# Optimization experiments

Measured on AMD Instinct MI355X. Metric: run time of the kernel, lower is better.

## Reference

```python
import jax, jax.numpy as jnp
import numpy as np

CAPACITY_FACTOR = 1.25

def setup_inputs() -> dict:
    key = jax.random.key(0)
    ks = jax.random.split(key, 6)
    B, S, D, H, E = 4, 2048, 1024, 2048, 8
    x = jax.random.normal(ks[0], (B, S, D), dtype=jnp.float32)
    Wg = jax.random.normal(ks[1], (D, E), dtype=jnp.float32) / np.float32(np.sqrt(D))
    bg = jnp.zeros((E,), dtype=jnp.float32)
    W1 = jax.random.normal(ks[2], (E, H, D), dtype=jnp.float32) / np.float32(np.sqrt(H))
    W2 = jax.random.normal(ks[3], (E, D, H), dtype=jnp.float32) / np.float32(np.sqrt(D))
    W3 = jax.random.normal(ks[4], (E, D, H), dtype=jnp.float32) / np.float32(np.sqrt(D))
    return {"x": x, "Wg": Wg, "bg": bg, "W1": W1, "W2": W2, "W3": W3, "deterministic": 1}


def reference(x, Wg, bg, W1, W2, W3, deterministic):
    # deterministic=True path: no gate noise, no dropout (rate=0 anyway).
    b, s, d = x.shape
    E = W1.shape[0]
    xt = x.reshape(-1, d)                      # [N, d]
    N = xt.shape[0]
    cap = int(N / E * CAPACITY_FACTOR)

    logits = xt @ Wg + bg                      # [N, E]
    eid = jnp.argmax(logits, axis=1)           # [N] assigned expert (top-1)
    onehot = jax.nn.one_hot(eid, E, dtype=xt.dtype)
    # 0-based arrival position of each token within its expert's queue
    pos = (jnp.sum(jnp.cumsum(onehot, axis=0) * onehot, axis=1)).astype(jnp.int32) - 1
    valid = pos < cap                          # capacity mask (pos >= 0 always)
    slot = jnp.where(valid, pos, cap)          # overflow tokens -> dummy slot `cap`

    # Dispatch: scatter tokens into [E, cap+1, d]; slots unique among valid tokens
    buf = jnp.zeros((E, cap + 1, d), dtype=xt.dtype).at[eid, slot].set(xt)
    binp = buf[:, :cap]                        # [E, cap, d] (dummy slot dropped)

    # Grouped SwiGLU FFN per expert
    h = jax.nn.silu(jnp.einsum('ecd,edh->ech', binp, W2)) * jnp.einsum('ecd,edh->ech', binp, W3)
    bout = jnp.einsum('ech,ehd->ecd', h, W1)   # [E, cap, d]

    # Combine: gather each token's expert output; overflow tokens read zero row
    bout = jnp.concatenate([bout, jnp.zeros((E, 1, d), dtype=bout.dtype)], axis=1)
    eout = bout[eid, slot]                     # [N, d]

    weights = jax.nn.softmax(logits, axis=-1)
    gate_w = jnp.take_along_axis(weights, eid[:, None], axis=1)  # [N, 1]
    out = (gate_w * eout).reshape(b, s, d)
    return out
```

## Files before the change

### kernel.cpp

```cpp
#include <hip/hip_runtime.h>

#define N_TOK 8192
#define D_DIM 1024
#define H_DIM 2048
#define E_NUM 8
#define CAP   1280

typedef __attribute__((ext_vector_type(8))) short bf16x8;
typedef __attribute__((ext_vector_type(8))) unsigned short u16x8;
typedef __attribute__((ext_vector_type(4))) float f32x4;

__device__ inline unsigned short f2bf(float f) {
  unsigned u = __float_as_uint(f);
  u += 0x7fffu + ((u >> 16) & 1u);
  return (unsigned short)(u >> 16);
}

__device__ inline void vm_drain() {
  asm volatile("s_waitcnt vmcnt(0)" ::: "memory");
}

__global__ __launch_bounds__(256) void transpose_cvt(const float* __restrict__ src,
                                                     unsigned short* __restrict__ dst,
                                                     int R, int C) {
  __shared__ float tile[64][33];
  const int b = blockIdx.z;
  src += (size_t)b * R * C;
  dst += (size_t)b * R * C;
  const int c0 = blockIdx.x * 32, r0 = blockIdx.y * 64;
  const int tx = threadIdx.x & 31, ty = threadIdx.x >> 5;
#pragma unroll
  for (int i = 0; i < 8; ++i)
    tile[ty + i * 8][tx] = src[(size_t)(r0 + ty + i * 8) * C + c0 + tx];
  __syncthreads();
  const int rp = threadIdx.x & 31;
  const int cb = threadIdx.x >> 5;
#pragma unroll
  for (int it = 0; it < 4; ++it) {
    const int c = cb + it * 8;
    unsigned short v[2] = {f2bf(tile[2 * rp][c]), f2bf(tile[2 * rp + 1][c])};
    *reinterpret_cast<unsigned*>(dst + (size_t)(c0 + c) * R + r0 + 2 * rp) =
        *reinterpret_cast<unsigned*>(v);
  }
}

__global__ __launch_bounds__(256) void gate_kernel(const float* __restrict__ x,
                                                   const float* __restrict__ Wg,
                                                   const float* __restrict__ bg,
                                                   int* __restrict__ eid,
                                                   float* __restrict__ gatew) {
  __shared__ float wg[E_NUM][D_DIM];
  const int tid = threadIdx.x;
  for (int i = tid; i < D_DIM * E_NUM; i += 256) {
    int d = i >> 3, e = i & 7;
    wg[e][d] = Wg[i];
  }
  __syncthreads();
  const int w = tid >> 6, l = tid & 63;
  const int t = blockIdx.x * 4 + w;
  const float* xr = x + (size_t)t * D_DIM;
  float acc[8] = {0, 0, 0, 0, 0, 0, 0, 0};
#pragma unroll
  for (int i = 0; i < D_DIM / 64; ++i) {
    float xv = xr[l + 64 * i];
#pragma unroll
    for (int e = 0; e < 8; ++e) acc[e] += xv * wg[e][l + 64 * i];
  }
#pragma unroll
  for (int off = 32; off >= 1; off >>= 1) {
#pragma unroll
    for (int e = 0; e < 8; ++e) acc[e] += __shfl_xor(acc[e], off);
  }
  if (l == 0) {
    float best = -1e30f;
    int bi = 0;
#pragma unroll
    for (int e = 0; e < 8; ++e) {
      acc[e] += bg[e];
      if (acc[e] > best) { best = acc[e]; bi = e; }
    }
    float s = 0.f;
#pragma unroll
    for (int e = 0; e < 8; ++e) s += __expf(acc[e] - best);
    eid[t] = bi;
    gatew[t] = 1.f / s;
  }
}

__global__ void init_tok(int* __restrict__ tok_of) {
  int i = blockIdx.x * 256 + threadIdx.x;
  if (i < E_NUM * CAP) tok_of[i] = -1;
}

__global__ void scan_kernel(const int* __restrict__ eid, int* __restrict__ slot,
                            int* __restrict__ tok_of) {
  __shared__ int se[N_TOK];
  const int tid = threadIdx.x;
  for (int i = tid; i < N_TOK; i += 256) se[i] = eid[i];
  __syncthreads();
  if (tid >= 64) return;
  int counts[8] = {0, 0, 0, 0, 0, 0, 0, 0};
  const unsigned long long lower = (tid == 0) ? 0ull : ((1ull << tid) - 1ull);
  for (int base = 0; base < N_TOK; base += 64) {
    const int t = base + tid;
    const int e = se[t];
    int rank = 0;
#pragma unroll
    for (int ee = 0; ee < 8; ++ee) {
      unsigned long long m = __ballot(e == ee);
      if (e == ee) rank = counts[ee] + __popcll(m & lower);
      counts[ee] += __popcll(m);
    }
    slot[t] = rank < CAP ? rank : CAP;
    if (rank < CAP) tok_of[e * CAP + rank] = t;
  }
}

__global__ __launch_bounds__(256) void scatter_kernel(const float* __restrict__ x,
                                                      const int* __restrict__ tok_of,
                                                      unsigned short* __restrict__ binp) {
  const int row = blockIdx.x * 4 + (threadIdx.x >> 6);
  const int l = threadIdx.x & 63;
  const int t = tok_of[row];
  unsigned short* dst = binp + (size_t)row * D_DIM;
  if (t >= 0) {
    const float* src = x + (size_t)t * D_DIM;
#pragma unroll
    for (int i = 0; i < 4; ++i) {
      const int d = (i * 64 + l) * 4;
      float4 v = *reinterpret_cast<const float4*>(src + d);
      unsigned short r[4] = {f2bf(v.x), f2bf(v.y), f2bf(v.z), f2bf(v.w)};
      *reinterpret_cast<uint2*>(dst + d) = *reinterpret_cast<uint2*>(r);
    }
  } else {
    uint2 z = {0u, 0u};
#pragma unroll
    for (int i = 0; i < 4; ++i) {
      const int d = (i * 64 + l) * 4;
      *reinterpret_cast<uint2*>(dst + d) = z;
    }
  }
}

__device__ inline void stage_tile_async(const unsigned short* __restrict__ g, int ldg, int k0,
                                        unsigned short* lds, int w, int l) {
  const int gcol = (l & 7) ^ (l >> 3);
  const unsigned short* gsrc = g + (size_t)(w * 32 + (l >> 3)) * ldg + k0 + gcol * 8;
#pragma unroll
  for (int it = 0; it < 4; ++it) {
    __builtin_amdgcn_global_load_lds(
        (const __attribute__((address_space(1))) unsigned int*)(gsrc + (size_t)(it * 8) * ldg),
        (__attribute__((address_space(3))) unsigned int*)(lds + (w * 32 + it * 8) * 64),
        16, 0, 0);
  }
}

__device__ inline bf16x8 lds_frag(const unsigned short* lds, int row, int c16) {
  return *reinterpret_cast<const bf16x8*>(lds + row * 64 + (c16 ^ (row & 7)) * 8);
}

__global__ __launch_bounds__(256, 2) void ffn1_kernel(const unsigned short* __restrict__ binp,
                                                      const unsigned short* __restrict__ w2t,
                                                      const unsigned short* __restrict__ w3t,
                                                      unsigned short* __restrict__ hbuf) {
  __shared__ unsigned short sA[128 * 64], sB2[128 * 64], sB3[128 * 64];
  const int e = blockIdx.z;
  const unsigned short* A  = binp + (size_t)e * CAP * D_DIM + (size_t)blockIdx.y * 128 * D_DIM;
  const unsigned short* B2 = w2t + (size_t)e * H_DIM * D_DIM + (size_t)blockIdx.x * 128 * D_DIM;
  const unsigned short* B3 = w3t + (size_t)e * H_DIM * D_DIM + (size_t)blockIdx.x * 128 * D_DIM;
  unsigned short* H = hbuf + (size_t)e * CAP * H_DIM;
  const int tid = threadIdx.x;
  const int l = tid & 63;
  const int w = tid >> 6, wr = w >> 1, wc = w & 1;
  f32x4 acc2[4][4] = {};
  f32x4 acc3[4][4] = {};
  for (int kt = 0; kt < D_DIM / 64; ++kt) {
    __syncthreads();
    stage_tile_async(A, D_DIM, kt * 64, sA, w, l);
    stage_tile_async(B2, D_DIM, kt * 64, sB2, w, l);
    stage_tile_async(B3, D_DIM, kt * 64, sB3, w, l);
    vm_drain();
    __syncthreads();
#pragma unroll
    for (int kk = 0; kk < 2; ++kk) {
      const int c16 = kk * 4 + (l >> 4);
      bf16x8 af[4], b2f[4], b3f[4];
#pragma unroll
      for (int f = 0; f < 4; ++f) {
        af[f] = lds_frag(sA, wr * 64 + f * 16 + (l & 15), c16);
        b2f[f] = lds_frag(sB2, wc * 64 + f * 16 + (l & 15), c16);
        b3f[f] = lds_frag(sB3, wc * 64 + f * 16 + (l & 15), c16);
      }
#pragma unroll
      for (int fm = 0; fm < 4; ++fm)
#pragma unroll
        for (int fn = 0; fn < 4; ++fn) {
          acc2[fm][fn] = __builtin_amdgcn_mfma_f32_16x16x32_bf16(af[fm], b2f[fn], acc2[fm][fn], 0, 0, 0);
          acc3[fm][fn] = __builtin_amdgcn_mfma_f32_16x16x32_bf16(af[fm], b3f[fn], acc3[fm][fn], 0, 0, 0);
        }
    }
  }
  const int row0 = blockIdx.y * 128 + wr * 64;
  const int col0 = blockIdx.x * 128 + wc * 64;
#pragma unroll
  for (int fm = 0; fm < 4; ++fm)
#pragma unroll
    for (int fn = 0; fn < 4; ++fn)
#pragma unroll
      for (int j = 0; j < 4; ++j) {
        const int row = row0 + fm * 16 + (l >> 4) * 4 + j;
        const int col = col0 + fn * 16 + (l & 15);
        const float v1 = acc2[fm][fn][j];
        const float v2 = acc3[fm][fn][j];
        const float hv = (v1 / (1.0f + __expf(-v1))) * v2;
        H[(size_t)row * H_DIM + col] = f2bf(hv);
      }
}

__global__ __launch_bounds__(256, 2) void ffn2_kernel(const unsigned short* __restrict__ hbuf,
                                                      const unsigned short* __restrict__ w1t,
                                                      const int* __restrict__ tok_of,
                                                      const float* __restrict__ gatew,
                                                      float* __restrict__ out) {
  __shared__ unsigned short sA[128 * 64], sB[128 * 64];
  const int e = blockIdx.z;
  const unsigned short* A = hbuf + (size_t)e * CAP * H_DIM + (size_t)blockIdx.y * 128 * H_DIM;
  const unsigned short* B = w1t + (size_t)e * D_DIM * H_DIM + (size_t)blockIdx.x * 128 * H_DIM;
  const int* tok = tok_of + e * CAP;
  const int tid = threadIdx.x;
  const int l = tid & 63;
  const int w = tid >> 6, wr = w >> 1, wc = w & 1;
  f32x4 acc[4][4] = {};
  for (int kt = 0; kt < H_DIM / 64; ++kt) {
    __syncthreads();
    stage_tile_async(A, H_DIM, kt * 64, sA, w, l);
    stage_tile_async(B, H_DIM, kt * 64, sB, w, l);
    vm_drain();
    __syncthreads();
#pragma unroll
    for (int kk = 0; kk < 2; ++kk) {
      const int c16 = kk * 4 + (l >> 4);
      bf16x8 af[4], bf[4];
#pragma unroll
      for (int f = 0; f < 4; ++f) {
        af[f] = lds_frag(sA, wr * 64 + f * 16 + (l & 15), c16);
        bf[f] = lds_frag(sB, wc * 64 + f * 16 + (l & 15), c16);
      }
#pragma unroll
      for (int fm = 0; fm < 4; ++fm)
#pragma unroll
        for (int fn = 0; fn < 4; ++fn)
          acc[fm][fn] = __builtin_amdgcn_mfma_f32_16x16x32_bf16(af[fm], bf[fn], acc[fm][fn], 0, 0, 0);
    }
  }
  const int row0 = blockIdx.y * 128 + wr * 64;
  const int col0 = blockIdx.x * 128 + wc * 64;
#pragma unroll
  for (int fm = 0; fm < 4; ++fm)
#pragma unroll
    for (int j = 0; j < 4; ++j) {
      const int row = row0 + fm * 16 + (l >> 4) * 4 + j;
      const int t = tok[row];
      if (t >= 0) {
        const float g = gatew[t];
#pragma unroll
        for (int fn = 0; fn < 4; ++fn) {
          const int col = col0 + fn * 16 + (l & 15);
          out[(size_t)t * D_DIM + col] = g * acc[fm][fn][j];
        }
      }
    }
}

__global__ __launch_bounds__(256) void zero_overflow(const int* __restrict__ slot,
                                                     float* __restrict__ out) {
  const int t = blockIdx.x * 4 + (threadIdx.x >> 6);
  if (slot[t] < CAP) return;
  const int l = threadIdx.x & 63;
  float4 z = {0.f, 0.f, 0.f, 0.f};
#pragma unroll
  for (int i = 0; i < 4; ++i)
    *reinterpret_cast<float4*>(out + (size_t)t * D_DIM + (i * 64 + l) * 4) = z;
}

extern "C" void kernel_launch(void* const* d_in, const int* in_sizes, int n_in,
                              void* d_out, int out_size, void* d_ws, size_t ws_size,
                              hipStream_t stream) {
  const float* x  = (const float*)d_in[0];
  const float* Wg = (const float*)d_in[1];
  const float* bg = (const float*)d_in[2];
  const float* W1 = (const float*)d_in[3];
  const float* W2 = (const float*)d_in[4];
  const float* W3 = (const float*)d_in[5];
  float* out = (float*)d_out;

  char* ws = (char*)d_ws;
  unsigned short* w2t = (unsigned short*)ws; ws += (size_t)E_NUM * H_DIM * D_DIM * 2;
  unsigned short* w3t = (unsigned short*)ws; ws += (size_t)E_NUM * H_DIM * D_DIM * 2;
  unsigned short* w1t = (unsigned short*)ws; ws += (size_t)E_NUM * D_DIM * H_DIM * 2;
  unsigned short* binp = (unsigned short*)ws; ws += (size_t)E_NUM * CAP * D_DIM * 2;
  unsigned short* hbuf = (unsigned short*)ws; ws += (size_t)E_NUM * CAP * H_DIM * 2;
  int* eid = (int*)ws;    ws += (size_t)N_TOK * 4;
  float* gw = (float*)ws; ws += (size_t)N_TOK * 4;
  int* slot = (int*)ws;   ws += (size_t)N_TOK * 4;
  int* tok_of = (int*)ws; ws += (size_t)E_NUM * CAP * 4;

  dim3 tb(256);
  transpose_cvt<<<dim3(H_DIM / 32, D_DIM / 64, E_NUM), tb, 0, stream>>>(W2, w2t, D_DIM, H_DIM);
  transpose_cvt<<<dim3(H_DIM / 32, D_DIM / 64, E_NUM), tb, 0, stream>>>(W3, w3t, D_DIM, H_DIM);
  transpose_cvt<<<dim3(D_DIM / 32, H_DIM / 64, E_NUM), tb, 0, stream>>>(W1, w1t, H_DIM, D_DIM);

  init_tok<<<(E_NUM * CAP + 255) / 256, 256, 0, stream>>>(tok_of);
  gate_kernel<<<N_TOK / 4, 256, 0, stream>>>(x, Wg, bg, eid, gw);
  scan_kernel<<<1, 256, 0, stream>>>(eid, slot, tok_of);
  scatter_kernel<<<E_NUM * CAP / 4, 256, 0, stream>>>(x, tok_of, binp);
  ffn1_kernel<<<dim3(H_DIM / 128, CAP / 128, E_NUM), 256, 0, stream>>>(binp, w2t, w3t, hbuf);
  ffn2_kernel<<<dim3(D_DIM / 128, CAP / 128, E_NUM), 256, 0, stream>>>(hbuf, w1t, tok_of, gw, out);
  zero_overflow<<<N_TOK / 4, 256, 0, stream>>>(slot, out);
}
```

Measured before the change: 272.7 us.

## Double-buffer LDS tiles with K=32 steps to overlap loads and MFMA

Both grouped GEMM kernels now split K into 32-wide tiles held in two LDS buffers, with a new XOR swizzle suited to the 32-column rows. The loads for the next tile are issued before the MFMAs on the current one, so global-to-LDS traffic overlaps compute instead of being drained before each step. The price is twice as many K iterations and barriers per output tile, with a shorter compute window to hide each load in.

Measured after the change: 327.8 us. 1.2x slower.

```diff
diff --git a/kernel.cpp b/kernel.cpp
--- a/kernel.cpp
+++ b/kernel.cpp
@@ -7,7 +7,6 @@
 #define CAP   1280
 
 typedef __attribute__((ext_vector_type(8))) short bf16x8;
-typedef __attribute__((ext_vector_type(8))) unsigned short u16x8;
 typedef __attribute__((ext_vector_type(4))) float f32x4;
 
 __device__ inline unsigned short f2bf(float f) {
@@ -142,28 +141,32 @@
   }
 }
 
-__device__ inline void stage_tile_async(const unsigned short* __restrict__ g, int ldg, int k0,
-                                        unsigned short* lds, int w, int l) {
-  const int gcol = (l & 7) ^ (l >> 3);
-  const unsigned short* gsrc = g + (size_t)(w * 32 + (l >> 3)) * ldg + k0 + gcol * 8;
-#pragma unroll
-  for (int it = 0; it < 4; ++it) {
+#define TILE32 (128 * 32)
+
+__device__ inline void stage_tile32(const unsigned short* __restrict__ g, int ldg, int k0,
+                                    unsigned short* lds, int w, int l) {
+  const int q = l >> 2;
+  const int gcol = (l & 3) ^ (q & 3) ^ ((q >> 2) & 3);
+  const unsigned short* gsrc = g + (size_t)(w * 32 + q) * ldg + k0 + gcol * 8;
+#pragma unroll
+  for (int it = 0; it < 2; ++it) {
     __builtin_amdgcn_global_load_lds(
-        (const __attribute__((address_space(1))) unsigned int*)(gsrc + (size_t)(it * 8) * ldg),
-        (__attribute__((address_space(3))) unsigned int*)(lds + (w * 32 + it * 8) * 64),
+        (const __attribute__((address_space(1))) unsigned int*)(gsrc + (size_t)(it * 16) * ldg),
+        (__attribute__((address_space(3))) unsigned int*)(lds + (w * 32 + it * 16) * 32),
         16, 0, 0);
   }
 }
 
-__device__ inline bf16x8 lds_frag(const unsigned short* lds, int row, int c16) {
-  return *reinterpret_cast<const bf16x8*>(lds + row * 64 + (c16 ^ (row & 7)) * 8);
+__device__ inline bf16x8 lds_frag32(const unsigned short* lds, int row, int c) {
+  const int ch = c ^ (row & 3) ^ ((row >> 2) & 3);
+  return *reinterpret_cast<const bf16x8*>(lds + row * 32 + ch * 8);
 }
 
 __global__ __launch_bounds__(256, 2) void ffn1_kernel(const unsigned short* __restrict__ binp,
                                                       const unsigned short* __restrict__ w2t,
                                                       const unsigned short* __restrict__ w3t,
                                                       unsigned short* __restrict__ hbuf) {
-  __shared__ unsigned short sA[128 * 64], sB2[128 * 64], sB3[128 * 64];
+  __shared__ unsigned short sA[2][TILE32], sB2[2][TILE32], sB3[2][TILE32];
   const int e = blockIdx.z;
   const unsigned short* A  = binp + (size_t)e * CAP * D_DIM + (size_t)blockIdx.y * 128 * D_DIM;
   const unsigned short* B2 = w2t + (size_t)e * H_DIM * D_DIM + (size_t)blockIdx.x * 128 * D_DIM;
@@ -174,32 +177,42 @@
   const int w = tid >> 6, wr = w >> 1, wc = w & 1;
   f32x4 acc2[4][4] = {};
   f32x4 acc3[4][4] = {};
-  for (int kt = 0; kt < D_DIM / 64; ++kt) {
-    __syncthreads();
-    stage_tile_async(A, D_DIM, kt * 64, sA, w, l);
-    stage_tile_async(B2, D_DIM, kt * 64, sB2, w, l);
-    stage_tile_async(B3, D_DIM, kt * 64, sB3, w, l);
+
+  stage_tile32(A, D_DIM, 0, sA[0], w, l);
+  stage_tile32(B2, D_DIM, 0, sB2[0], w, l);
+  stage_tile32(B3, D_DIM, 0, sB3[0], w, l);
+  vm_drain();
+  __syncthreads();
+
+  const int NT = D_DIM / 32;
+  int cur = 0;
+  for (int kt = 0; kt < NT; ++kt) {
+    const int nxt = cur ^ 1;
+    if (kt + 1 < NT) {
+      stage_tile32(A, D_DIM, (kt + 1) * 32, sA[nxt], w, l);
+      stage_tile32(B2, D_DIM, (kt + 1) * 32, sB2[nxt], w, l);
+      stage_tile32(B3, D_DIM, (kt + 1) * 32, sB3[nxt], w, l);
+    }
+    const int c = l >> 4;
+    bf16x8 af[4], b2f[4], b3f[4];
+#pragma unroll
+    for (int f = 0; f < 4; ++f) {
+      af[f]  = lds_frag32(sA[cur],  wr * 64 + f * 16 + (l & 15), c);
+      b2f[f] = lds_frag32(sB2[cur], wc * 64 + f * 16 + (l & 15), c);
+      b3f[f] = lds_frag32(sB3[cur], wc * 64 + f * 16 + (l & 15), c);
+    }
+#pragma unroll
+    for (int fm = 0; fm < 4; ++fm)
+#pragma unroll
+      for (int fn = 0; fn < 4; ++fn) {
+        acc2[fm][fn] = __builtin_amdgcn_mfma_f32_16x16x32_bf16(af[fm], b2f[fn], acc2[fm][fn], 0, 0, 0);
+        acc3[fm][fn] = __builtin_amdgcn_mfma_f32_16x16x32_bf16(af[fm], b3f[fn], acc3[fm][fn], 0, 0, 0);
+      }
     vm_drain();
     __syncthreads();
-#pragma unroll
-    for (int kk = 0; kk < 2; ++kk) {
-      const int c16 = kk * 4 + (l >> 4);
-      bf16x8 af[4], b2f[4], b3f[4];
-#pragma unroll
-      for (int f = 0; f < 4; ++f) {
-        af[f] = lds_frag(sA, wr * 64 + f * 16 + (l & 15), c16);
-        b2f[f] = lds_frag(sB2, wc * 64 + f * 16 + (l & 15), c16);
-        b3f[f] = lds_frag(sB3, wc * 64 + f * 16 + (l & 15), c16);
-      }
-#pragma unroll
-      for (int fm = 0; fm < 4; ++fm)
-#pragma unroll
-        for (int fn = 0; fn < 4; ++fn) {
-          acc2[fm][fn] = __builtin_amdgcn_mfma_f32_16x16x32_bf16(af[fm], b2f[fn], acc2[fm][fn], 0, 0, 0);
-          acc3[fm][fn] = __builtin_amdgcn_mfma_f32_16x16x32_bf16(af[fm], b3f[fn], acc3[fm][fn], 0, 0, 0);
-        }
-    }
-  }
+    cur = nxt;
+  }
+
   const int row0 = blockIdx.y * 128 + wr * 64;
   const int col0 = blockIdx.x * 128 + wc * 64;
 #pragma unroll
@@ -222,7 +235,7 @@
                                                       const int* __restrict__ tok_of,
                                                       const float* __restrict__ gatew,
                                                       float* __restrict__ out) {
-  __shared__ unsigned short sA[128 * 64], sB[128 * 64];
+  __shared__ unsigned short sA[2][TILE32], sB[2][TILE32];
   const int e = blockIdx.z;
   const unsigned short* A = hbuf + (size_t)e * CAP * H_DIM + (size_t)blockIdx.y * 128 * H_DIM;
   const unsigned short* B = w1t + (size_t)e * D_DIM * H_DIM + (size_t)blockIdx.x * 128 * H_DIM;
@@ -231,28 +244,37 @@
   const int l = tid & 63;
   const int w = tid >> 6, wr = w >> 1, wc = w & 1;
   f32x4 acc[4][4] = {};
-  for (int kt = 0; kt < H_DIM / 64; ++kt) {
-    __syncthreads();
-    stage_tile_async(A, H_DIM, kt * 64, sA, w, l);
-    stage_tile_async(B, H_DIM, kt * 64, sB, w, l);
+
+  stage_tile32(A, H_DIM, 0, sA[0], w, l);
+  stage_tile32(B, H_DIM, 0, sB[0], w, l);
+  vm_drain();
+  __syncthreads();
+
+  const int NT = H_DIM / 32;
+  int cur = 0;
+  for (int kt = 0; kt < NT; ++kt) {
+    const int nxt = cur ^ 1;
+    if (kt + 1 < NT) {
+      stage_tile32(A, H_DIM, (kt + 1) * 32, sA[nxt], w, l);
+      stage_tile32(B, H_DIM, (kt + 1) * 32, sB[nxt], w, l);
+    }
+    const int c = l >> 4;
+    bf16x8 af[4], bfr[4];
+#pragma unroll
+    for (int f = 0; f < 4; ++f) {
+      af[f]  = lds_frag32(sA[cur], wr * 64 + f * 16 + (l & 15), c);
+      bfr[f] = lds_frag32(sB[cur], wc * 64 + f * 16 + (l & 15), c);
+    }
+#pragma unroll
+    for (int fm = 0; fm < 4; ++fm)
+#pragma unroll
+      for (int fn = 0; fn < 4; ++fn)
+        acc[fm][fn] = __builtin_amdgcn_mfma_f32_16x16x32_bf16(af[fm], bfr[fn], acc[fm][fn], 0, 0, 0);
     vm_drain();
     __syncthreads();
-#pragma unroll
-    for (int kk = 0; kk < 2; ++kk) {
-      const int c16 = kk * 4 + (l >> 4);
-      bf16x8 af[4], bf[4];
-#pragma unroll
-      for (int f = 0; f < 4; ++f) {
-        af[f] = lds_frag(sA, wr * 64 + f * 16 + (l & 15), c16);
-        bf[f] = lds_frag(sB, wc * 64 + f * 16 + (l & 15), c16);
-      }
-#pragma unroll
-      for (int fm = 0; fm < 4; ++fm)
-#pragma unroll
-        for (int fn = 0; fn < 4; ++fn)
-          acc[fm][fn] = __builtin_amdgcn_mfma_f32_16x16x32_bf16(af[fm], bf[fn], acc[fm][fn], 0, 0, 0);
-    }
-  }
+    cur = nxt;
+  }
+
   const int row0 = blockIdx.y * 128 + wr * 64;
   const int col0 = blockIdx.x * 128 + wc * 64;
 #pragma unroll
```

## Double-buffer GEMM K-loop and interleave W2/W3 into one B operand

Applied to the files above, without the earlier changes.

Both FFN GEMMs now use double-buffered LDS tiles: the next K slice is prefetched with async global-to-LDS loads while MFMAs run on the current slice, which hides load latency behind compute. The gate and up projection weights are packed into one interleaved matrix, 64 rows of W2 followed by 64 rows of W3 per 128-row block. ffn1 therefore computes one 128x128 output tile, and the SwiGLU pairing is done through an LDS scratch exchange between wave columns. This halves ffn1's accumulator registers and doubles its grid, at the cost of an extra LDS round trip in the epilogue and more LDS per block.

Result: slower. 290.3 us (+6.4%).

```diff
diff --git a/kernel.cpp b/kernel.cpp
--- a/kernel.cpp
+++ b/kernel.cpp
@@ -7,7 +7,6 @@
 #define CAP   1280
 
 typedef __attribute__((ext_vector_type(8))) short bf16x8;
-typedef __attribute__((ext_vector_type(8))) unsigned short u16x8;
 typedef __attribute__((ext_vector_type(4))) float f32x4;
 
 __device__ inline unsigned short f2bf(float f) {
@@ -40,6 +39,32 @@
     const int c = cb + it * 8;
     unsigned short v[2] = {f2bf(tile[2 * rp][c]), f2bf(tile[2 * rp + 1][c])};
     *reinterpret_cast<unsigned*>(dst + (size_t)(c0 + c) * R + r0 + 2 * rp) =
+        *reinterpret_cast<unsigned*>(v);
+  }
+}
+
+__global__ __launch_bounds__(256) void transpose_cvt_merge(const float* __restrict__ src,
+                                                           unsigned short* __restrict__ dst,
+                                                           int R, int C, int rowoff) {
+  __shared__ float tile[64][33];
+  const int b = blockIdx.z;
+  src += (size_t)b * R * C;
+  dst += (size_t)b * 2 * C * R;
+  const int c0 = blockIdx.x * 32, r0 = blockIdx.y * 64;
+  const int tx = threadIdx.x & 31, ty = threadIdx.x >> 5;
+#pragma unroll
+  for (int i = 0; i < 8; ++i)
+    tile[ty + i * 8][tx] = src[(size_t)(r0 + ty + i * 8) * C + c0 + tx];
+  __syncthreads();
+  const int rp = threadIdx.x & 31;
+  const int cb = threadIdx.x >> 5;
+#pragma unroll
+  for (int it = 0; it < 4; ++it) {
+    const int c = cb + it * 8;
+    const int h = c0 + c;
+    const size_t drow = (size_t)(h >> 6) * 128 + (h & 63) + rowoff;
+    unsigned short v[2] = {f2bf(tile[2 * rp][c]), f2bf(tile[2 * rp + 1][c])};
+    *reinterpret_cast<unsigned*>(dst + drow * R + r0 + 2 * rp) =
         *reinterpret_cast<unsigned*>(v);
   }
 }
@@ -142,8 +167,10 @@
   }
 }
 
-__device__ inline void stage_tile_async(const unsigned short* __restrict__ g, int ldg, int k0,
-                                        unsigned short* lds, int w, int l) {
+#define TILE64 (128 * 64)
+
+__device__ inline void stage_tile(const unsigned short* __restrict__ g, int ldg, int k0,
+                                  unsigned short* lds, int w, int l) {
   const int gcol = (l & 7) ^ (l >> 3);
   const unsigned short* gsrc = g + (size_t)(w * 32 + (l >> 3)) * ldg + k0 + gcol * 8;
 #pragma unroll
@@ -160,61 +187,82 @@
 }
 
 __global__ __launch_bounds__(256, 2) void ffn1_kernel(const unsigned short* __restrict__ binp,
-                                                      const unsigned short* __restrict__ w2t,
-                                                      const unsigned short* __restrict__ w3t,
+                                                      const unsigned short* __restrict__ wq,
                                                       unsigned short* __restrict__ hbuf) {
-  __shared__ unsigned short sA[128 * 64], sB2[128 * 64], sB3[128 * 64];
-  const int e = blockIdx.z;
-  const unsigned short* A  = binp + (size_t)e * CAP * D_DIM + (size_t)blockIdx.y * 128 * D_DIM;
-  const unsigned short* B2 = w2t + (size_t)e * H_DIM * D_DIM + (size_t)blockIdx.x * 128 * D_DIM;
-  const unsigned short* B3 = w3t + (size_t)e * H_DIM * D_DIM + (size_t)blockIdx.x * 128 * D_DIM;
+  __shared__ unsigned short sb[2][2][TILE64];
+  const int e = blockIdx.z, bx = blockIdx.x, by = blockIdx.y;
+  const unsigned short* A = binp + (size_t)e * CAP * D_DIM + (size_t)by * 128 * D_DIM;
+  const unsigned short* B = wq + ((size_t)e * (H_DIM / 64) + bx) * 128 * D_DIM;
   unsigned short* H = hbuf + (size_t)e * CAP * H_DIM;
   const int tid = threadIdx.x;
   const int l = tid & 63;
   const int w = tid >> 6, wr = w >> 1, wc = w & 1;
-  f32x4 acc2[4][4] = {};
-  f32x4 acc3[4][4] = {};
-  for (int kt = 0; kt < D_DIM / 64; ++kt) {
-    __syncthreads();
-    stage_tile_async(A, D_DIM, kt * 64, sA, w, l);
-    stage_tile_async(B2, D_DIM, kt * 64, sB2, w, l);
-    stage_tile_async(B3, D_DIM, kt * 64, sB3, w, l);
+  f32x4 acc[4][4] = {};
+
+  stage_tile(A, D_DIM, 0, sb[0][0], w, l);
+  stage_tile(B, D_DIM, 0, sb[0][1], w, l);
+  vm_drain();
+  __syncthreads();
+
+  const int NT = D_DIM / 64;
+  int cur = 0;
+  for (int kt = 0; kt < NT; ++kt) {
+    const int nxt = cur ^ 1;
+    if (kt + 1 < NT) {
+      stage_tile(A, D_DIM, (kt + 1) * 64, sb[nxt][0], w, l);
+      stage_tile(B, D_DIM, (kt + 1) * 64, sb[nxt][1], w, l);
+    }
+#pragma unroll
+    for (int kk = 0; kk < 2; ++kk) {
+      const int c16 = kk * 4 + (l >> 4);
+      bf16x8 af[4], bfr[4];
+#pragma unroll
+      for (int f = 0; f < 4; ++f) {
+        af[f]  = lds_frag(sb[cur][0], wr * 64 + f * 16 + (l & 15), c16);
+        bfr[f] = lds_frag(sb[cur][1], wc * 64 + f * 16 + (l & 15), c16);
+      }
+#pragma unroll
+      for (int fm = 0; fm < 4; ++fm)
+#pragma unroll
+        for (int fn = 0; fn < 4; ++fn)
+          acc[fm][fn] = __builtin_amdgcn_mfma_f32_16x16x32_bf16(af[fm], bfr[fn], acc[fm][fn], 0, 0, 0);
+    }
     vm_drain();
     __syncthreads();
-#pragma unroll
-    for (int kk = 0; kk < 2; ++kk) {
-      const int c16 = kk * 4 + (l >> 4);
-      bf16x8 af[4], b2f[4], b3f[4];
-#pragma unroll
-      for (int f = 0; f < 4; ++f) {
-        af[f] = lds_frag(sA, wr * 64 + f * 16 + (l & 15), c16);
-        b2f[f] = lds_frag(sB2, wc * 64 + f * 16 + (l & 15), c16);
-        b3f[f] = lds_frag(sB3, wc * 64 + f * 16 + (l & 15), c16);
-      }
-#pragma unroll
-      for (int fm = 0; fm < 4; ++fm)
-#pragma unroll
-        for (int fn = 0; fn < 4; ++fn) {
-          acc2[fm][fn] = __builtin_amdgcn_mfma_f32_16x16x32_bf16(af[fm], b2f[fn], acc2[fm][fn], 0, 0, 0);
-          acc3[fm][fn] = __builtin_amdgcn_mfma_f32_16x16x32_bf16(af[fm], b3f[fn], acc3[fm][fn], 0, 0, 0);
+    cur = nxt;
+  }
+
+  float* scr = reinterpret_cast<float*>(&sb[0][0][0]);
+  if (wc == 1) {
+#pragma unroll
+    for (int fm = 0; fm < 4; ++fm)
+#pragma unroll
+      for (int fn = 0; fn < 4; ++fn)
+#pragma unroll
+        for (int j = 0; j < 4; ++j) {
+          const int r = fm * 16 + (l >> 4) * 4 + j;
+          const int c = fn * 16 + (l & 15);
+          scr[wr * 4160 + r * 65 + c] = acc[fm][fn][j];
         }
-    }
-  }
-  const int row0 = blockIdx.y * 128 + wr * 64;
-  const int col0 = blockIdx.x * 128 + wc * 64;
-#pragma unroll
-  for (int fm = 0; fm < 4; ++fm)
-#pragma unroll
-    for (int fn = 0; fn < 4; ++fn)
-#pragma unroll
-      for (int j = 0; j < 4; ++j) {
-        const int row = row0 + fm * 16 + (l >> 4) * 4 + j;
-        const int col = col0 + fn * 16 + (l & 15);
-        const float v1 = acc2[fm][fn][j];
-        const float v2 = acc3[fm][fn][j];
-        const float hv = (v1 / (1.0f + __expf(-v1))) * v2;
-        H[(size_t)row * H_DIM + col] = f2bf(hv);
-      }
+  }
+  __syncthreads();
+  if (wc == 0) {
+    const int row0 = by * 128 + wr * 64;
+    const int col0 = bx * 64;
+#pragma unroll
+    for (int fm = 0; fm < 4; ++fm)
+#pragma unroll
+      for (int fn = 0; fn < 4; ++fn)
+#pragma unroll
+        for (int j = 0; j < 4; ++j) {
+          const int r = fm * 16 + (l >> 4) * 4 + j;
+          const int c = fn * 16 + (l & 15);
+          const float v2 = acc[fm][fn][j];
+          const float v3 = scr[wr * 4160 + r * 65 + c];
+          const float hv = (v2 / (1.0f + __expf(-v2))) * v3;
+          H[(size_t)(row0 + r) * H_DIM + col0 + c] = f2bf(hv);
+        }
+  }
 }
 
 __global__ __launch_bounds__(256, 2) void ffn2_kernel(const unsigned short* __restrict__ hbuf,
@@ -222,7 +270,7 @@
                                                       const int* __restrict__ tok_of,
                                                       const float* __restrict__ gatew,
                                                       float* __restrict__ out) {
-  __shared__ unsigned short sA[128 * 64], sB[128 * 64];
+  __shared__ unsigned short sb[2][2][TILE64];
   const int e = blockIdx.z;
   const unsigned short* A = hbuf + (size_t)e * CAP * H_DIM + (size_t)blockIdx.y * 128 * H_DIM;
   const unsigned short* B = w1t + (size_t)e * D_DIM * H_DIM + (size_t)blockIdx.x * 128 * H_DIM;
@@ -231,28 +279,40 @@
   const int l = tid & 63;
   const int w = tid >> 6, wr = w >> 1, wc = w & 1;
   f32x4 acc[4][4] = {};
-  for (int kt = 0; kt < H_DIM / 64; ++kt) {
-    __syncthreads();
-    stage_tile_async(A, H_DIM, kt * 64, sA, w, l);
-    stage_tile_async(B, H_DIM, kt * 64, sB, w, l);
+
+  stage_tile(A, H_DIM, 0, sb[0][0], w, l);
+  stage_tile(B, H_DIM, 0, sb[0][1], w, l);
+  vm_drain();
+  __syncthreads();
+
+  const int NT = H_DIM / 64;
+  int cur = 0;
+  for (int kt = 0; kt < NT; ++kt) {
+    const int nxt = cur ^ 1;
+    if (kt + 1 < NT) {
+      stage_tile(A, H_DIM, (kt + 1) * 64, sb[nxt][0], w, l);
+      stage_tile(B, H_DIM, (kt + 1) * 64, sb[nxt][1], w, l);
+    }
+#pragma unroll
+    for (int kk = 0; kk < 2; ++kk) {
+      const int c16 = kk * 4 + (l >> 4);
+      bf16x8 af[4], bfr[4];
+#pragma unroll
+      for (int f = 0; f < 4; ++f) {
+        af[f]  = lds_frag(sb[cur][0], wr * 64 + f * 16 + (l & 15), c16);
+        bfr[f] = lds_frag(sb[cur][1], wc * 64 + f * 16 + (l & 15), c16);
+      }
+#pragma unroll
+      for (int fm = 0; fm < 4; ++fm)
+#pragma unroll
+        for (int fn = 0; fn < 4; ++fn)
+          acc[fm][fn] = __builtin_amdgcn_mfma_f32_16x16x32_bf16(af[fm], bfr[fn], acc[fm][fn], 0, 0, 0);
+    }
     vm_drain();
     __syncthreads();
-#pragma unroll
-    for (int kk = 0; kk < 2; ++kk) {
-      const int c16 = kk * 4 + (l >> 4);
-      bf16x8 af[4], bf[4];
-#pragma unroll
-      for (int f = 0; f < 4; ++f) {
-        af[f] = lds_frag(sA, wr * 64 + f * 16 + (l & 15), c16);
-        bf[f] = lds_frag(sB, wc * 64 + f * 16 + (l & 15), c16);
-      }
-#pragma unroll
-      for (int fm = 0; fm < 4; ++fm)
-#pragma unroll
-        for (int fn = 0; fn < 4; ++fn)
-          acc[fm][fn] = __builtin_amdgcn_mfma_f32_16x16x32_bf16(af[fm], bf[fn], acc[fm][fn], 0, 0, 0);
-    }
-  }
+    cur = nxt;
+  }
+
   const int row0 = blockIdx.y * 128 + wr * 64;
   const int col0 = blockIdx.x * 128 + wc * 64;
 #pragma unroll
@@ -295,8 +355,7 @@
   float* out = (float*)d_out;
 
   char* ws = (char*)d_ws;
-  unsigned short* w2t = (unsigned short*)ws; ws += (size_t)E_NUM * H_DIM * D_DIM * 2;
-  unsigned short* w3t = (unsigned short*)ws; ws += (size_t)E_NUM * H_DIM * D_DIM * 2;
+  unsigned short* wq  = (unsigned short*)ws; ws += (size_t)E_NUM * 2 * H_DIM * D_DIM * 2;
   unsigned short* w1t = (unsigned short*)ws; ws += (size_t)E_NUM * D_DIM * H_DIM * 2;
   unsigned short* binp = (unsigned short*)ws; ws += (size_t)E_NUM * CAP * D_DIM * 2;
   unsigned short* hbuf = (unsigned short*)ws; ws += (size_t)E_NUM * CAP * H_DIM * 2;
@@ -306,15 +365,15 @@
   int* tok_of = (int*)ws; ws += (size_t)E_NUM * CAP * 4;
 
   dim3 tb(256);
-  transpose_cvt<<<dim3(H_DIM / 32, D_DIM / 64, E_NUM), tb, 0, stream>>>(W2, w2t, D_DIM, H_DIM);
-  transpose_cvt<<<dim3(H_DIM / 32, D_DIM / 64, E_NUM), tb, 0, stream>>>(W3, w3t, D_DIM, H_DIM);
+  transpose_cvt_merge<<<dim3(H_DIM / 32, D_DIM / 64, E_NUM), tb, 0, stream>>>(W2, wq, D_DIM, H_DIM, 0);
+  transpose_cvt_merge<<<dim3(H_DIM / 32, D_DIM / 64, E_NUM), tb, 0, stream>>>(W3, wq, D_DIM, H_DIM, 64);
   transpose_cvt<<<dim3(D_DIM / 32, H_DIM / 64, E_NUM), tb, 0, stream>>>(W1, w1t, H_DIM, D_DIM);
 
   init_tok<<<(E_NUM * CAP + 255) / 256, 256, 0, stream>>>(tok_of);
   gate_kernel<<<N_TOK / 4, 256, 0, stream>>>(x, Wg, bg, eid, gw);
   scan_kernel<<<1, 256, 0, stream>>>(eid, slot, tok_of);
   scatter_kernel<<<E_NUM * CAP / 4, 256, 0, stream>>>(x, tok_of, binp);
-  ffn1_kernel<<<dim3(H_DIM / 128, CAP / 128, E_NUM), 256, 0, stream>>>(binp, w2t, w3t, hbuf);
+  ffn1_kernel<<<dim3(H_DIM / 64, CAP / 128, E_NUM), 256, 0, stream>>>(binp, wq, hbuf);
   ffn2_kernel<<<dim3(D_DIM / 128, CAP / 128, E_NUM), 256, 0, stream>>>(hbuf, w1t, tok_of, gw, out);
   zero_overflow<<<N_TOK / 4, 256, 0, stream>>>(slot, out);
 }
```

## Pre-tile weights into MFMA fragment layout and load B directly from global

Applied to the files above, without the earlier changes.

The weight transpose kernel now writes bf16 weights in a fragment-major layout, so each lane can read its MFMA B operand with one 16-byte global load and the weight tiles no longer pass through LDS. Only the activation tile is staged in LDS, now double-buffered so the next tile loads while MFMAs run on the current one. FFN2 switches to 128-thread blocks where each wave covers 64 rows by 128 columns, and the init kernel is replaced by a memset. The cost is more global load traffic and register pressure for B fragments in exchange for fewer LDS writes and barriers, with a risk of exposed global latency.

After: 294.6 us. 8.0% more time.

```diff
diff --git a/kernel.cpp b/kernel.cpp
--- a/kernel.cpp
+++ b/kernel.cpp
@@ -7,7 +7,6 @@
 #define CAP   1280
 
 typedef __attribute__((ext_vector_type(8))) short bf16x8;
-typedef __attribute__((ext_vector_type(8))) unsigned short u16x8;
 typedef __attribute__((ext_vector_type(4))) float f32x4;
 
 __device__ inline unsigned short f2bf(float f) {
@@ -20,9 +19,9 @@
   asm volatile("s_waitcnt vmcnt(0)" ::: "memory");
 }
 
-__global__ __launch_bounds__(256) void transpose_cvt(const float* __restrict__ src,
-                                                     unsigned short* __restrict__ dst,
-                                                     int R, int C) {
+__global__ __launch_bounds__(256) void transpose_cvt_frag(const float* __restrict__ src,
+                                                          unsigned short* __restrict__ dst,
+                                                          int R, int C) {
   __shared__ float tile[64][33];
   const int b = blockIdx.z;
   src += (size_t)b * R * C;
@@ -33,15 +32,14 @@
   for (int i = 0; i < 8; ++i)
     tile[ty + i * 8][tx] = src[(size_t)(r0 + ty + i * 8) * C + c0 + tx];
   __syncthreads();
-  const int rp = threadIdx.x & 31;
-  const int cb = threadIdx.x >> 5;
-#pragma unroll
-  for (int it = 0; it < 4; ++it) {
-    const int c = cb + it * 8;
-    unsigned short v[2] = {f2bf(tile[2 * rp][c]), f2bf(tile[2 * rp + 1][c])};
-    *reinterpret_cast<unsigned*>(dst + (size_t)(c0 + c) * R + r0 + 2 * rp) =
-        *reinterpret_cast<unsigned*>(v);
-  }
+  const int c = threadIdx.x & 31;
+  const int ro = threadIdx.x >> 5;
+  unsigned short v[8];
+#pragma unroll
+  for (int i = 0; i < 8; ++i) v[i] = f2bf(tile[ro * 8 + i][c]);
+  const int gc = c0 + c;
+  const size_t off = ((size_t)(gc >> 4) * (R >> 3) + (r0 >> 3) + ro) * 128 + (gc & 15) * 8;
+  *reinterpret_cast<bf16x8*>(dst + off) = *reinterpret_cast<const bf16x8*>(v);
 }
 
 __global__ __launch_bounds__(256) void gate_kernel(const float* __restrict__ x,
@@ -87,11 +85,6 @@
   }
 }
 
-__global__ void init_tok(int* __restrict__ tok_of) {
-  int i = blockIdx.x * 256 + threadIdx.x;
-  if (i < E_NUM * CAP) tok_of[i] = -1;
-}
-
 __global__ void scan_kernel(const int* __restrict__ eid, int* __restrict__ slot,
                             int* __restrict__ tok_of) {
   __shared__ int se[N_TOK];
@@ -142,8 +135,10 @@
   }
 }
 
-__device__ inline void stage_tile_async(const unsigned short* __restrict__ g, int ldg, int k0,
-                                        unsigned short* lds, int w, int l) {
+#define TILE64 (128 * 64)
+
+__device__ inline void stage_tile4(const unsigned short* __restrict__ g, int ldg, int k0,
+                                   unsigned short* lds, int w, int l) {
   const int gcol = (l & 7) ^ (l >> 3);
   const unsigned short* gsrc = g + (size_t)(w * 32 + (l >> 3)) * ldg + k0 + gcol * 8;
 #pragma unroll
@@ -155,53 +150,85 @@
   }
 }
 
+__device__ inline void stage_tile2(const unsigned short* __restrict__ g, int ldg, int k0,
+                                   unsigned short* lds, int w, int l) {
+  const int gcol = (l & 7) ^ (l >> 3);
+  const unsigned short* gsrc = g + (size_t)(w * 64 + (l >> 3)) * ldg + k0 + gcol * 8;
+#pragma unroll
+  for (int it = 0; it < 8; ++it) {
+    __builtin_amdgcn_global_load_lds(
+        (const __attribute__((address_space(1))) unsigned int*)(gsrc + (size_t)(it * 8) * ldg),
+        (__attribute__((address_space(3))) unsigned int*)(lds + (w * 64 + it * 8) * 64),
+        16, 0, 0);
+  }
+}
+
 __device__ inline bf16x8 lds_frag(const unsigned short* lds, int row, int c16) {
   return *reinterpret_cast<const bf16x8*>(lds + row * 64 + (c16 ^ (row & 7)) * 8);
 }
 
+__device__ inline bf16x8 gfrag(const unsigned short* __restrict__ wf, int n16, int kcb,
+                               int KD8, int l) {
+  return *reinterpret_cast<const bf16x8*>(
+      wf + ((size_t)n16 * KD8 + kcb + (l >> 4)) * 128 + (l & 15) * 8);
+}
+
 __global__ __launch_bounds__(256, 2) void ffn1_kernel(const unsigned short* __restrict__ binp,
-                                                      const unsigned short* __restrict__ w2t,
-                                                      const unsigned short* __restrict__ w3t,
+                                                      const unsigned short* __restrict__ w2f,
+                                                      const unsigned short* __restrict__ w3f,
                                                       unsigned short* __restrict__ hbuf) {
-  __shared__ unsigned short sA[128 * 64], sB2[128 * 64], sB3[128 * 64];
-  const int e = blockIdx.z;
-  const unsigned short* A  = binp + (size_t)e * CAP * D_DIM + (size_t)blockIdx.y * 128 * D_DIM;
-  const unsigned short* B2 = w2t + (size_t)e * H_DIM * D_DIM + (size_t)blockIdx.x * 128 * D_DIM;
-  const unsigned short* B3 = w3t + (size_t)e * H_DIM * D_DIM + (size_t)blockIdx.x * 128 * D_DIM;
+  __shared__ unsigned short sA[2][TILE64];
+  const int e = blockIdx.z, bx = blockIdx.x, by = blockIdx.y;
+  const unsigned short* A = binp + (size_t)e * CAP * D_DIM + (size_t)by * 128 * D_DIM;
+  const unsigned short* B2 = w2f + (size_t)e * H_DIM * D_DIM;
+  const unsigned short* B3 = w3f + (size_t)e * H_DIM * D_DIM;
   unsigned short* H = hbuf + (size_t)e * CAP * H_DIM;
   const int tid = threadIdx.x;
   const int l = tid & 63;
   const int w = tid >> 6, wr = w >> 1, wc = w & 1;
+  const int h16w = bx * 8 + wc * 4;
   f32x4 acc2[4][4] = {};
   f32x4 acc3[4][4] = {};
-  for (int kt = 0; kt < D_DIM / 64; ++kt) {
-    __syncthreads();
-    stage_tile_async(A, D_DIM, kt * 64, sA, w, l);
-    stage_tile_async(B2, D_DIM, kt * 64, sB2, w, l);
-    stage_tile_async(B3, D_DIM, kt * 64, sB3, w, l);
+
+  stage_tile4(A, D_DIM, 0, sA[0], w, l);
+  vm_drain();
+  __syncthreads();
+
+  const int NT = D_DIM / 64;
+  int cur = 0;
+  for (int kt = 0; kt < NT; ++kt) {
+    const int nxt = cur ^ 1;
+    bf16x8 b2[2][4], b3[2][4];
+#pragma unroll
+    for (int kk = 0; kk < 2; ++kk)
+#pragma unroll
+      for (int f = 0; f < 4; ++f) {
+        b2[kk][f] = gfrag(B2, h16w + f, kt * 8 + kk * 4, D_DIM / 8, l);
+        b3[kk][f] = gfrag(B3, h16w + f, kt * 8 + kk * 4, D_DIM / 8, l);
+      }
+    if (kt + 1 < NT) stage_tile4(A, D_DIM, (kt + 1) * 64, sA[nxt], w, l);
+#pragma unroll
+    for (int kk = 0; kk < 2; ++kk) {
+      const int c16 = kk * 4 + (l >> 4);
+      bf16x8 af[4];
+#pragma unroll
+      for (int f = 0; f < 4; ++f)
+        af[f] = lds_frag(sA[cur], wr * 64 + f * 16 + (l & 15), c16);
+#pragma unroll
+      for (int fm = 0; fm < 4; ++fm)
+#pragma unroll
+        for (int fn = 0; fn < 4; ++fn) {
+          acc2[fm][fn] = __builtin_amdgcn_mfma_f32_16x16x32_bf16(af[fm], b2[kk][fn], acc2[fm][fn], 0, 0, 0);
+          acc3[fm][fn] = __builtin_amdgcn_mfma_f32_16x16x32_bf16(af[fm], b3[kk][fn], acc3[fm][fn], 0, 0, 0);
+        }
+    }
     vm_drain();
     __syncthreads();
-#pragma unroll
-    for (int kk = 0; kk < 2; ++kk) {
-      const int c16 = kk * 4 + (l >> 4);
-      bf16x8 af[4], b2f[4], b3f[4];
-#pragma unroll
-      for (int f = 0; f < 4; ++f) {
-        af[f] = lds_frag(sA, wr * 64 + f * 16 + (l & 15), c16);
-        b2f[f] = lds_frag(sB2, wc * 64 + f * 16 + (l & 15), c16);
-        b3f[f] = lds_frag(sB3, wc * 64 + f * 16 + (l & 15), c16);
-      }
-#pragma unroll
-      for (int fm = 0; fm < 4; ++fm)
-#pragma unroll
-        for (int fn = 0; fn < 4; ++fn) {
-          acc2[fm][fn] = __builtin_amdgcn_mfma_f32_16x16x32_bf16(af[fm], b2f[fn], acc2[fm][fn], 0, 0, 0);
-          acc3[fm][fn] = __builtin_amdgcn_mfma_f32_16x16x32_bf16(af[fm], b3f[fn], acc3[fm][fn], 0, 0, 0);
-        }
-    }
-  }
-  const int row0 = blockIdx.y * 128 + wr * 64;
-  const int col0 = blockIdx.x * 128 + wc * 64;
+    cur = nxt;
+  }
+
+  const int row0 = by * 128 + wr * 64;
+  const int col0 = bx * 128 + wc * 64;
 #pragma unroll
   for (int fm = 0; fm < 4; ++fm)
 #pragma unroll
@@ -210,51 +237,64 @@
       for (int j = 0; j < 4; ++j) {
         const int row = row0 + fm * 16 + (l >> 4) * 4 + j;
         const int col = col0 + fn * 16 + (l & 15);
-        const float v1 = acc2[fm][fn][j];
-        const float v2 = acc3[fm][fn][j];
-        const float hv = (v1 / (1.0f + __expf(-v1))) * v2;
+        const float v2 = acc2[fm][fn][j];
+        const float v3 = acc3[fm][fn][j];
+        const float hv = (v2 / (1.0f + __expf(-v2))) * v3;
         H[(size_t)row * H_DIM + col] = f2bf(hv);
       }
 }
 
-__global__ __launch_bounds__(256, 2) void ffn2_kernel(const unsigned short* __restrict__ hbuf,
-                                                      const unsigned short* __restrict__ w1t,
+__global__ __launch_bounds__(128, 2) void ffn2_kernel(const unsigned short* __restrict__ hbuf,
+                                                      const unsigned short* __restrict__ w1f,
                                                       const int* __restrict__ tok_of,
                                                       const float* __restrict__ gatew,
                                                       float* __restrict__ out) {
-  __shared__ unsigned short sA[128 * 64], sB[128 * 64];
-  const int e = blockIdx.z;
-  const unsigned short* A = hbuf + (size_t)e * CAP * H_DIM + (size_t)blockIdx.y * 128 * H_DIM;
-  const unsigned short* B = w1t + (size_t)e * D_DIM * H_DIM + (size_t)blockIdx.x * 128 * H_DIM;
+  __shared__ unsigned short sA[2][TILE64];
+  const int e = blockIdx.z, bx = blockIdx.x, by = blockIdx.y;
+  const unsigned short* A = hbuf + (size_t)e * CAP * H_DIM + (size_t)by * 128 * H_DIM;
+  const unsigned short* B = w1f + (size_t)e * D_DIM * H_DIM;
   const int* tok = tok_of + e * CAP;
   const int tid = threadIdx.x;
   const int l = tid & 63;
-  const int w = tid >> 6, wr = w >> 1, wc = w & 1;
-  f32x4 acc[4][4] = {};
-  for (int kt = 0; kt < H_DIM / 64; ++kt) {
-    __syncthreads();
-    stage_tile_async(A, H_DIM, kt * 64, sA, w, l);
-    stage_tile_async(B, H_DIM, kt * 64, sB, w, l);
+  const int w = tid >> 6;
+  const int d16w = bx * 8;
+  f32x4 acc[4][8] = {};
+
+  stage_tile2(A, H_DIM, 0, sA[0], w, l);
+  vm_drain();
+  __syncthreads();
+
+  const int NT = H_DIM / 64;
+  int cur = 0;
+  for (int kt = 0; kt < NT; ++kt) {
+    const int nxt = cur ^ 1;
+    bf16x8 bfr[2][8];
+#pragma unroll
+    for (int kk = 0; kk < 2; ++kk)
+#pragma unroll
+      for (int fn = 0; fn < 8; ++fn)
+        bfr[kk][fn] = gfrag(B, d16w + fn, kt * 8 + kk * 4, H_DIM / 8, l);
+    if (kt + 1 < NT) stage_tile2(A, H_DIM, (kt + 1) * 64, sA[nxt], w, l);
+#pragma unroll
+    for (int kk = 0; kk < 2; ++kk) {
+      const int c16 = kk * 4 + (l >> 4);
+      bf16x8 af[4];
+#pragma unroll
+      for (int f = 0; f < 4; ++f)
+        af[f] = lds_frag(sA[cur], w * 64 + f * 16 + (l & 15), c16);
+#pragma unroll
+      for (int fm = 0; fm < 4; ++fm)
+#pragma unroll
+        for (int fn = 0; fn < 8; ++fn)
+          acc[fm][fn] = __builtin_amdgcn_mfma_f32_16x16x32_bf16(af[fm], bfr[kk][fn], acc[fm][fn], 0, 0, 0);
+    }
     vm_drain();
     __syncthreads();
-#pragma unroll
-    for (int kk = 0; kk < 2; ++kk) {
-      const int c16 = kk * 4 + (l >> 4);
-      bf16x8 af[4], bf[4];
-#pragma unroll
-      for (int f = 0; f < 4; ++f) {
-        af[f] = lds_frag(sA, wr * 64 + f * 16 + (l & 15), c16);
-        bf[f] = lds_frag(sB, wc * 64 + f * 16 + (l & 15), c16);
-      }
-#pragma unroll
-      for (int fm = 0; fm < 4; ++fm)
-#pragma unroll
-        for (int fn = 0; fn < 4; ++fn)
-          acc[fm][fn] = __builtin_amdgcn_mfma_f32_16x16x32_bf16(af[fm], bf[fn], acc[fm][fn], 0, 0, 0);
-    }
-  }
-  const int row0 = blockIdx.y * 128 + wr * 64;
-  const int col0 = blockIdx.x * 128 + wc * 64;
+    cur = nxt;
+  }
+
+  const int row0 = by * 128 + w * 64;
+  const int col0 = bx * 128;
 #pragma unroll
   for (int fm = 0; fm < 4; ++fm)
 #pragma unroll
@@ -264,7 +304,7 @@
       if (t >= 0) {
         const float g = gatew[t];
 #pragma unroll
-        for (int fn = 0; fn < 4; ++fn) {
+        for (int fn = 0; fn < 8; ++fn) {
           const int col = col0 + fn * 16 + (l & 15);
           out[(size_t)t * D_DIM + col] = g * acc[fm][fn][j];
         }
@@ -295,9 +335,9 @@
   float* out = (float*)d_out;
 
   char* ws = (char*)d_ws;
-  unsigned short* w2t = (unsigned short*)ws; ws += (size_t)E_NUM * H_DIM * D_DIM * 2;
-  unsigned short* w3t = (unsigned short*)ws; ws += (size_t)E_NUM * H_DIM * D_DIM * 2;
-  unsigned short* w1t = (unsigned short*)ws; ws += (size_t)E_NUM * D_DIM * H_DIM * 2;
+  unsigned short* w2f = (unsigned short*)ws; ws += (size_t)E_NUM * H_DIM * D_DIM * 2;
+  unsigned short* w3f = (unsigned short*)ws; ws += (size_t)E_NUM * H_DIM * D_DIM * 2;
+  unsigned short* w1f = (unsigned short*)ws; ws += (size_t)E_NUM * D_DIM * H_DIM * 2;
   unsigned short* binp = (unsigned short*)ws; ws += (size_t)E_NUM * CAP * D_DIM * 2;
   unsigned short* hbuf = (unsigned short*)ws; ws += (size_t)E_NUM * CAP * H_DIM * 2;
   int* eid = (int*)ws;    ws += (size_t)N_TOK * 4;
@@ -306,15 +346,15 @@
   int* tok_of = (int*)ws; ws += (size_t)E_NUM * CAP * 4;
 
   dim3 tb(256);
-  transpose_cvt<<<dim3(H_DIM / 32, D_DIM / 64, E_NUM), tb, 0, stream>>>(W2, w2t, D_DIM, H_DIM);
-  transpose_cvt<<<dim3(H_DIM / 32, D_DIM / 64, E_NUM), tb, 0, stream>>>(W3, w3t, D_DIM, H_DIM);
-  transpose_cvt<<<dim3(D_DIM / 32, H_DIM / 64, E_NUM), tb, 0, stream>>>(W1, w1t, H_DIM, D_DIM);
-
-  init_tok<<<(E_NUM * CAP + 255) / 256, 256, 0, stream>>>(tok_of);
+  transpose_cvt_frag<<<dim3(H_DIM / 32, D_DIM / 64, E_NUM), tb, 0, stream>>>(W2, w2f, D_DIM, H_DIM);
+  transpose_cvt_frag<<<dim3(H_DIM / 32, D_DIM / 64, E_NUM), tb, 0, stream>>>(W3, w3f, D_DIM, H_DIM);
+  transpose_cvt_frag<<<dim3(D_DIM / 32, H_DIM / 64, E_NUM), tb, 0, stream>>>(W1, w1f, H_DIM, D_DIM);
+
+  hipMemsetAsync(tok_of, 0xFF, (size_t)E_NUM * CAP * 4, stream);
   gate_kernel<<<N_TOK / 4, 256, 0, stream>>>(x, Wg, bg, eid, gw);
   scan_kernel<<<1, 256, 0, stream>>>(eid, slot, tok_of);
   scatter_kernel<<<E_NUM * CAP / 4, 256, 0, stream>>>(x, tok_of, binp);
-  ffn1_kernel<<<dim3(H_DIM / 128, CAP / 128, E_NUM), 256, 0, stream>>>(binp, w2t, w3t, hbuf);
-  ffn2_kernel<<<dim3(D_DIM / 128, CAP / 128, E_NUM), 256, 0, stream>>>(hbuf, w1t, tok_of, gw, out);
+  ffn1_kernel<<<dim3(H_DIM / 128, CAP / 128, E_NUM), 256, 0, stream>>>(binp, w2f, w3f, hbuf);
+  ffn2_kernel<<<dim3(D_DIM / 128, CAP / 128, E_NUM), 128, 0, stream>>>(hbuf, w1f, tok_of, gw, out);
   zero_overflow<<<N_TOK / 4, 256, 0, stream>>>(slot, out);
 }
```
